# Kernel optimization log

Measured on AMD Instinct MI355X. Metric: run time of the kernel, lower is better.

Reference implementation:

```python
import jax, jax.numpy as jnp
import numpy as np

C_S, C_Z, N_HEADS = 768, 64, 12
HEAD_DIM = C_S // N_HEADS
L = 1024
EPS = 1e-5


def _ln(x, g, b):
    mu = jnp.mean(x, axis=-1, keepdims=True)
    var = jnp.mean((x - mu) ** 2, axis=-1, keepdims=True)
    return (x - mu) * jax.lax.rsqrt(var + EPS) * g + b


def setup_inputs() -> dict:
    key = jax.random.key(0)
    ks = jax.random.split(key, 12)
    w = lambda k, shp, fan_in: jax.random.normal(k, shp, dtype=jnp.float32) / np.sqrt(fan_in)
    return {
        "single": jax.random.normal(ks[0], (L, C_S), dtype=jnp.float32),
        "pair": jax.random.normal(ks[1], (L, L, C_Z), dtype=jnp.float32),
        "ln_s_g": jnp.ones((C_S,), jnp.float32),
        "ln_s_b": jnp.zeros((C_S,), jnp.float32),
        "ln_z_g": jnp.ones((C_Z,), jnp.float32),
        "ln_z_b": jnp.zeros((C_Z,), jnp.float32),
        "Wq": w(ks[2], (C_S, C_S), C_S),
        "Wk": w(ks[3], (C_S, C_S), C_S),
        "Wv": w(ks[4], (C_S, C_S), C_S),
        "Wb": w(ks[5], (C_Z, N_HEADS), C_Z),
        "Wout": w(ks[6], (C_S, C_S), C_S),
        "bout": jnp.zeros((C_S,), jnp.float32),
        "Wgate": w(ks[7], (C_S, C_S), C_S),
        "bgate": jnp.zeros((C_S,), jnp.float32),
    }


def reference(single, pair, ln_s_g, ln_s_b, ln_z_g, ln_z_b,
              Wq, Wk, Wv, Wb, Wout, bout, Wgate, bgate):
    Lq = single.shape[0]
    s = _ln(single, ln_s_g, ln_s_b)                    # [L, C_S]
    z = _ln(pair, ln_z_g, ln_z_b)                      # [L, L, C_Z]
    q = (s @ Wq).reshape(Lq, N_HEADS, HEAD_DIM)
    k = (s @ Wk).reshape(Lq, N_HEADS, HEAD_DIM)
    v = (s @ Wv).reshape(Lq, N_HEADS, HEAD_DIM)
    logits = jnp.einsum('ihd,jhd->hij', q, k) / np.sqrt(HEAD_DIM)
    logits = logits + jnp.einsum('ijc,ch->hij', z, Wb)  # pair bias per head
    attn = jax.nn.softmax(logits, axis=-1)              # [H, L, L]
    out = jnp.einsum('hij,jhd->ihd', attn, v).reshape(Lq, C_S)
    return single + jax.nn.sigmoid(s @ Wgate + bgate) * (out @ Wout + bout)
```

## Files before the change

### kernel.cpp

```cpp
#include <hip/hip_runtime.h>

#define LQ 1024
#define CS 768
#define CZ 64
#define NH 12
#define HD 64

typedef float4 f4;
using bf16x8 = __attribute__((ext_vector_type(8))) short;
using f32x4  = __attribute__((ext_vector_type(4))) float;

static __device__ __forceinline__ unsigned short f2bf(float f) {
  unsigned int u = __float_as_uint(f);
  u += 0x7fffu + ((u >> 16) & 1u);
  return (unsigned short)(u >> 16);
}
static __device__ __forceinline__ float bf2f(unsigned short b) {
  return __uint_as_float(((unsigned int)b) << 16);
}
static __device__ __forceinline__ unsigned cvtpk(float lo, float hi) {
  unsigned r;
  asm("v_cvt_pk_bf16_f32 %0, %1, %2" : "=v"(r) : "v"(lo), "v"(hi));
  return r;
}

__global__ __launch_bounds__(256) void ln_wconv_k(
    const float* __restrict__ x, const float* __restrict__ g,
    const float* __restrict__ b, unsigned short* __restrict__ s_out,
    const float* __restrict__ Wq, const float* __restrict__ Wk,
    const float* __restrict__ Wv, const float* __restrict__ Wg,
    const float* __restrict__ Wo, unsigned short* __restrict__ wt) {
  const int bid = blockIdx.x;
  const int t = threadIdx.x;
  if (bid < LQ) {
    const int row = bid;
    const float* xr = x + (size_t)row * CS;
    float v0 = xr[t], v1 = xr[t + 256], v2 = xr[t + 512];
    float s1 = v0 + v1 + v2;
    float s2 = v0 * v0 + v1 * v1 + v2 * v2;
#pragma unroll
    for (int m = 1; m < 64; m <<= 1) {
      s1 += __shfl_xor(s1, m);
      s2 += __shfl_xor(s2, m);
    }
    __shared__ float r1[4], r2[4];
    const int wid = t >> 6;
    if ((t & 63) == 0) { r1[wid] = s1; r2[wid] = s2; }
    __syncthreads();
    s1 = r1[0] + r1[1] + r1[2] + r1[3];
    s2 = r2[0] + r2[1] + r2[2] + r2[3];
    const float mu = s1 * (1.f / CS);
    const float var = s2 * (1.f / CS) - mu * mu;
    const float rs = rsqrtf(var + 1e-5f);
    s_out[(size_t)row * CS + t]       = f2bf((v0 - mu) * rs * g[t]       + b[t]);
    s_out[(size_t)row * CS + t + 256] = f2bf((v1 - mu) * rs * g[t + 256] + b[t + 256]);
    s_out[(size_t)row * CS + t + 512] = f2bf((v2 - mu) * rs * g[t + 512] + b[t + 512]);
  } else {
    int r = bid - LQ;
    const int bz = r / 144; r %= 144;
    const int n0 = (r % 12) * 64, k0 = (r / 12) * 64;
    const float* W;
    switch (bz) {
      case 0: W = Wq; break;
      case 1: W = Wk; break;
      case 2: W = Wv; break;
      case 3: W = Wg; break;
      default: W = Wo; break;
    }
    unsigned short* o = wt + (size_t)bz * CS * CS;
    __shared__ float T[64][68];
    {
      const int rr = t >> 4, c = (t & 15) * 4;
#pragma unroll
      for (int u = 0; u < 4; ++u) {
        const f4 v = *(const f4*)&W[(size_t)(k0 + rr + u * 16) * CS + n0 + c];
        *(f4*)&T[rr + u * 16][c] = v;
      }
    }
    __syncthreads();
    {
      const int rn = t >> 2, ck = (t & 3) * 16;
      __align__(16) unsigned short tmp[16];
#pragma unroll
      for (int u = 0; u < 16; ++u) tmp[u] = f2bf(T[ck + u][rn]);
      unsigned short* dst = &o[(size_t)(n0 + rn) * CS + k0 + ck];
      *(uint4*)dst = ((const uint4*)tmp)[0];
      *(uint4*)(dst + 8) = ((const uint4*)tmp)[1];
    }
  }
}

__global__ __launch_bounds__(256) void pair_k(
    const float* __restrict__ pair, const float* __restrict__ zg,
    const float* __restrict__ zb, const float* __restrict__ Wb,
    unsigned short* __restrict__ biasF) {
  __shared__ __align__(16) unsigned short outT[12 * 520 + 8];
  const int bid = blockIdx.x;
  const int t = threadIdx.x;
  const int w = t >> 6, lane = t & 63, g = lane >> 4, c = lane & 15;
  const int i0 = (bid >> 3) * 4;
  const int j0 = (bid & 7) * 128;
  const int il = c & 3, jl = c >> 2;
  const int irow = i0 + il;
  const int g2 = g * 2;

  const int csafe = (c < NH) ? c : 0;
  float C1 = 0.f, C2 = 0.f;
  for (int ch = 0; ch < CZ; ++ch) {
    const float wv = (c < NH) ? Wb[ch * NH + csafe] : 0.f;
    C1 = fmaf(zg[ch], wv, C1);
    C2 = fmaf(zb[ch], wv, C2);
  }
  bf16x8 wf0, wf1;
#pragma unroll
  for (int u = 0; u < 8; ++u) {
    const float w0 = (c < NH) ? zg[g * 8 + u] * Wb[(g * 8 + u) * NH + csafe] : 0.f;
    const float w1 = (c < NH) ? zg[32 + g * 8 + u] * Wb[(32 + g * 8 + u) * NH + csafe] : 0.f;
    wf0[u] = (short)f2bf(w0);
    wf1[u] = (short)f2bf(w1);
  }

  f32x4 p00, p01, p02, p03;
  f32x4 p10, p11, p12, p13;
  {
    const f32x4* s0 = (const f32x4*)(pair + ((size_t)irow * LQ + (j0 + w * 32 + jl)) * CZ);
    p00 = s0[g2]; p01 = s0[g2 + 1]; p02 = s0[g2 + 8]; p03 = s0[g2 + 9];
  }
#pragma unroll
  for (int it = 0; it < 8; ++it) {
    const bool useA = (it & 1) == 0;
    if (it < 7) {
      const f32x4* sn = (const f32x4*)(pair + ((size_t)irow * LQ + (j0 + w * 32 + (it + 1) * 4 + jl)) * CZ);
      if (useA) { p10 = sn[g2]; p11 = sn[g2 + 1]; p12 = sn[g2 + 8]; p13 = sn[g2 + 9]; }
      else      { p00 = sn[g2]; p01 = sn[g2 + 1]; p02 = sn[g2 + 8]; p03 = sn[g2 + 9]; }
    }
    const f32x4 x0a = useA ? p00 : p10;
    const f32x4 x0b = useA ? p01 : p11;
    const f32x4 x1a = useA ? p02 : p12;
    const f32x4 x1b = useA ? p03 : p13;

    float s1 = (((x0a[0] + x0a[1]) + (x0a[2] + x0a[3])) + ((x0b[0] + x0b[1]) + (x0b[2] + x0b[3])))
             + (((x1a[0] + x1a[1]) + (x1a[2] + x1a[3])) + ((x1b[0] + x1b[1]) + (x1b[2] + x1b[3])));
    float s2 = (((x0a[0]*x0a[0] + x0a[1]*x0a[1]) + (x0a[2]*x0a[2] + x0a[3]*x0a[3]))
             +  ((x0b[0]*x0b[0] + x0b[1]*x0b[1]) + (x0b[2]*x0b[2] + x0b[3]*x0b[3])))
             + (((x1a[0]*x1a[0] + x1a[1]*x1a[1]) + (x1a[2]*x1a[2] + x1a[3]*x1a[3]))
             +  ((x1b[0]*x1b[0] + x1b[1]*x1b[1]) + (x1b[2]*x1b[2] + x1b[3]*x1b[3])));
    s1 += __shfl_xor(s1, 16); s1 += __shfl_xor(s1, 32);
    s2 += __shfl_xor(s2, 16); s2 += __shfl_xor(s2, 32);
    const float mu = s1 * (1.f / CZ);
    const float var = s2 * (1.f / CZ) - mu * mu;
    const float rs = rsqrtf(var + 1e-5f);
    const float mup = -rs * mu;

    union { unsigned u[4]; bf16x8 v8; } A, B;
    A.u[0] = cvtpk(x0a[0], x0a[1]); A.u[1] = cvtpk(x0a[2], x0a[3]);
    A.u[2] = cvtpk(x0b[0], x0b[1]); A.u[3] = cvtpk(x0b[2], x0b[3]);
    B.u[0] = cvtpk(x1a[0], x1a[1]); B.u[1] = cvtpk(x1a[2], x1a[3]);
    B.u[2] = cvtpk(x1b[0], x1b[1]); B.u[3] = cvtpk(x1b[2], x1b[3]);

    f32x4 dd = (f32x4){0.f, 0.f, 0.f, 0.f};
    dd = __builtin_amdgcn_mfma_f32_16x16x32_bf16(A.v8, wf0, dd, 0, 0, 0);
    dd = __builtin_amdgcn_mfma_f32_16x16x32_bf16(B.v8, wf1, dd, 0, 0, 0);

    const float rr0 = __shfl(rs, g * 4 + 0), mm0 = __shfl(mup, g * 4 + 0);
    const float rr1 = __shfl(rs, g * 4 + 1), mm1 = __shfl(mup, g * 4 + 1);
    const float rr2 = __shfl(rs, g * 4 + 2), mm2 = __shfl(mup, g * 4 + 2);
    const float rr3 = __shfl(rs, g * 4 + 3), mm3 = __shfl(mup, g * 4 + 3);

    if (c < NH) {
      const float b0 = fmaf(rr0, dd[0], fmaf(mm0, C1, C2));
      const float b1 = fmaf(rr1, dd[1], fmaf(mm1, C1, C2));
      const float b2 = fmaf(rr2, dd[2], fmaf(mm2, C1, C2));
      const float b3 = fmaf(rr3, dd[3], fmaf(mm3, C1, C2));
      const int jrel = w * 32 + it * 4 + g;
      const int s = jrel >> 4;
      uint2 st;
      st.x = cvtpk(b0, b1);
      st.y = cvtpk(b2, b3);
      *(uint2*)&outT[c * 520 + s * 64 + (jrel & 15) * 4] = st;
    }
  }
  __syncthreads();

  const int gi = i0 >> 4, ga = (i0 >> 2) & 3;
#pragma unroll
  for (int rep = 0; rep < 3; ++rep) {
    const int idx = rep * 256 + t;
    const int hh = idx >> 6;
    const int s = (idx >> 3) & 7;
    const int sub = idx & 7;
    const uint4 v = *(const uint4*)&outT[hh * 520 + s * 64 + sub * 8];
    const size_t flat = ((((size_t)hh * 64 + gi) * 16 + (j0 >> 6) + (s >> 2)) * 4 + (s & 3)) * 256
                      + (size_t)ga * 64 + sub * 8;
    *(uint4*)&biasF[flat] = v;
  }
}

__global__ __launch_bounds__(256) void gemm_qkvg_k(
    const unsigned short* __restrict__ s, const unsigned short* __restrict__ wt,
    const float* __restrict__ bg,
    unsigned short* __restrict__ qb, unsigned short* __restrict__ kb,
    unsigned short* __restrict__ vt, float* __restrict__ gpre) {
  __shared__ __align__(16) unsigned short As[64][88];
  __shared__ __align__(16) unsigned short Bs[128][88];
  const int t = threadIdx.x;
  const int w = t >> 6, lane = t & 63, g = lane >> 4, c = lane & 15;
  const int wm = w >> 1, wn = w & 1;
  const int bx = blockIdx.x % 24, by = blockIdx.x / 24;
  const int m0 = by * 64;
  const int wid = bx / 6;
  const int nl0 = (bx % 6) * 128;
  const unsigned short* B = wt + (size_t)wid * CS * CS;

  f32x4 acc[2][4];
#pragma unroll
  for (int i = 0; i < 2; ++i)
#pragma unroll
    for (int j = 0; j < 4; ++j) acc[i][j] = (f32x4){0.f, 0.f, 0.f, 0.f};

  const int sra = t >> 2, sha = (t & 3) * 16;
  const int srb = t >> 1, shb = (t & 1) * 32;
  for (int kt = 0; kt < CS; kt += 64) {
    __syncthreads();
#pragma unroll
    for (int u = 0; u < 2; ++u)
      *(uint4*)&As[sra][sha + u * 8] = *(const uint4*)&s[(size_t)(m0 + sra) * CS + kt + sha + u * 8];
#pragma unroll
    for (int u = 0; u < 4; ++u)
      *(uint4*)&Bs[srb][shb + u * 8] = *(const uint4*)&B[(size_t)(nl0 + srb) * CS + kt + shb + u * 8];
    __syncthreads();
#pragma unroll
    for (int kk = 0; kk < 64; kk += 32) {
      bf16x8 af[2], bfr[4];
#pragma unroll
      for (int i = 0; i < 2; ++i) af[i] = *(const bf16x8*)&As[wm * 32 + i * 16 + c][kk + g * 8];
#pragma unroll
      for (int j = 0; j < 4; ++j) bfr[j] = *(const bf16x8*)&Bs[wn * 64 + j * 16 + c][kk + g * 8];
#pragma unroll
      for (int i = 0; i < 2; ++i)
#pragma unroll
        for (int j = 0; j < 4; ++j)
          acc[i][j] = __builtin_amdgcn_mfma_f32_16x16x32_bf16(af[i], bfr[j], acc[i][j], 0, 0, 0);
    }
  }
#pragma unroll
  for (int i = 0; i < 2; ++i) {
#pragma unroll
    for (int j = 0; j < 4; ++j) {
      const int mb = m0 + wm * 32 + i * 16 + g * 4;
      const int nn = nl0 + wn * 64 + j * 16 + c;
      const f32x4 a = acc[i][j];
      if (wid == 0) {
#pragma unroll
        for (int r = 0; r < 4; ++r) qb[(size_t)(mb + r) * CS + nn] = f2bf(a[r] * 0.125f);
      } else if (wid == 1) {
#pragma unroll
        for (int r = 0; r < 4; ++r) kb[(size_t)(mb + r) * CS + nn] = f2bf(a[r]);
      } else if (wid == 2) {
        ushort4 pk;
        pk.x = f2bf(a[0]); pk.y = f2bf(a[1]); pk.z = f2bf(a[2]); pk.w = f2bf(a[3]);
        *(ushort4*)&vt[(size_t)nn * LQ + mb] = pk;
      } else {
        const float bb = bg[nn];
#pragma unroll
        for (int r = 0; r < 4; ++r) gpre[(size_t)(mb + r) * CS + nn] = a[r] + bb;
      }
    }
  }
}

__global__ __launch_bounds__(256) void attn_k(
    const unsigned short* __restrict__ q, const unsigned short* __restrict__ k,
    const unsigned short* __restrict__ vt, const unsigned short* __restrict__ biasF,
    float* __restrict__ Opart, float* __restrict__ ml) {
  __shared__ __align__(16) unsigned short Qs[64][88];
  __shared__ __align__(16) unsigned short Ks[2][64][88];
  __shared__ __align__(16) unsigned short Vts[2][64][88];
  __shared__ __align__(16) unsigned short Ps[4][16][88];
  const int bx = blockIdx.x, h = blockIdx.y, z = blockIdx.z;
  const int i0 = bx * 64;
  const int jb = z * 512;
  const int t = threadIdx.x;
  const int w = t >> 6, lane = t & 63, g = lane >> 4, c = lane & 15;
  const int sr = t >> 2, sc = (t & 3) * 16;

#pragma unroll
  for (int u = 0; u < 2; ++u) {
    *(uint4*)&Qs[sr][sc + u * 8]     = *(const uint4*)&q[(size_t)(i0 + sr) * CS + h * HD + sc + u * 8];
    *(uint4*)&Ks[0][sr][sc + u * 8]  = *(const uint4*)&k[(size_t)(jb + sr) * CS + h * HD + sc + u * 8];
    *(uint4*)&Vts[0][sr][sc + u * 8] = *(const uint4*)&vt[(size_t)(h * HD + sr) * LQ + jb + sc + u * 8];
  }
  const size_t bbase = ((((size_t)h * 64 + (bx * 4 + w)) * 16 + (size_t)z * 8) * 4) * 256 + lane * 4;
  ushort4 bcur[4];
#pragma unroll
  for (int nb = 0; nb < 4; ++nb) bcur[nb] = *(const ushort4*)&biasF[bbase + nb * 256];
  __syncthreads();

  const bf16x8 aq0 = *(const bf16x8*)&Qs[w * 16 + c][g * 8];
  const bf16x8 aq1 = *(const bf16x8*)&Qs[w * 16 + c][32 + g * 8];

  f32x4 acc_o[4];
#pragma unroll
  for (int nb = 0; nb < 4; ++nb) acc_o[nb] = (f32x4){0.f, 0.f, 0.f, 0.f};
  float m_run[4] = {-1e30f, -1e30f, -1e30f, -1e30f};
  float l_run[4] = {0.f, 0.f, 0.f, 0.f};

  for (int jt = 0; jt < 8; ++jt) {
    const int cur = jt & 1;
    uint4 kr0, kr1, vr0, vr1;
    ushort4 bnx[4];
    if (jt < 7) {
      const int jn = jb + (jt + 1) * 64;
      kr0 = *(const uint4*)&k[(size_t)(jn + sr) * CS + h * HD + sc];
      kr1 = *(const uint4*)&k[(size_t)(jn + sr) * CS + h * HD + sc + 8];
      vr0 = *(const uint4*)&vt[(size_t)(h * HD + sr) * LQ + jn + sc];
      vr1 = *(const uint4*)&vt[(size_t)(h * HD + sr) * LQ + jn + sc + 8];
#pragma unroll
      for (int nb = 0; nb < 4; ++nb)
        bnx[nb] = *(const ushort4*)&biasF[bbase + (size_t)(jt + 1) * 1024 + nb * 256];
    }

    f32x4 sa[4];
#pragma unroll
    for (int nb = 0; nb < 4; ++nb) {
      f32x4 ci;
      ci[0] = bf2f(bcur[nb].x); ci[1] = bf2f(bcur[nb].y);
      ci[2] = bf2f(bcur[nb].z); ci[3] = bf2f(bcur[nb].w);
      const bf16x8 b0 = *(const bf16x8*)&Ks[cur][nb * 16 + c][g * 8];
      const bf16x8 b1 = *(const bf16x8*)&Ks[cur][nb * 16 + c][32 + g * 8];
      ci = __builtin_amdgcn_mfma_f32_16x16x32_bf16(aq0, b0, ci, 0, 0, 0);
      ci = __builtin_amdgcn_mfma_f32_16x16x32_bf16(aq1, b1, ci, 0, 0, 0);
      sa[nb] = ci;
    }

    float mt[4];
#pragma unroll
    for (int r = 0; r < 4; ++r) {
      float v = fmaxf(fmaxf(sa[0][r], sa[1][r]), fmaxf(sa[2][r], sa[3][r]));
      v = fmaxf(v, __shfl_xor(v, 1));
      v = fmaxf(v, __shfl_xor(v, 2));
      v = fmaxf(v, __shfl_xor(v, 4));
      v = fmaxf(v, __shfl_xor(v, 8));
      mt[r] = v;
    }
    float scale[4], ps[4];
#pragma unroll
    for (int r = 0; r < 4; ++r) {
      const float mn = fmaxf(m_run[r], mt[r]);
      scale[r] = __expf(m_run[r] - mn);
      m_run[r] = mn;
      ps[r] = 0.f;
    }
#pragma unroll
    for (int nb = 0; nb < 4; ++nb) {
#pragma unroll
      for (int r = 0; r < 4; ++r) {
        const float p = __expf(sa[nb][r] - m_run[r]);
        ps[r] += p;
        Ps[w][g * 4 + r][nb * 16 + c] = f2bf(p);
      }
    }
#pragma unroll
    for (int r = 0; r < 4; ++r) {
      float v = ps[r];
      v += __shfl_xor(v, 1);
      v += __shfl_xor(v, 2);
      v += __shfl_xor(v, 4);
      v += __shfl_xor(v, 8);
      l_run[r] = l_run[r] * scale[r] + v;
#pragma unroll
      for (int nb = 0; nb < 4; ++nb) acc_o[nb][r] *= scale[r];
    }

#pragma unroll
    for (int kb = 0; kb < 2; ++kb) {
      const bf16x8 pa = *(const bf16x8*)&Ps[w][c][kb * 32 + g * 8];
#pragma unroll
      for (int nb = 0; nb < 4; ++nb) {
        const bf16x8 bv = *(const bf16x8*)&Vts[cur][nb * 16 + c][kb * 32 + g * 8];
        acc_o[nb] = __builtin_amdgcn_mfma_f32_16x16x32_bf16(pa, bv, acc_o[nb], 0, 0, 0);
      }
    }

    if (jt < 7) {
      *(uint4*)&Ks[cur ^ 1][sr][sc]      = kr0;
      *(uint4*)&Ks[cur ^ 1][sr][sc + 8]  = kr1;
      *(uint4*)&Vts[cur ^ 1][sr][sc]     = vr0;
      *(uint4*)&Vts[cur ^ 1][sr][sc + 8] = vr1;
      __syncthreads();
#pragma unroll
      for (int nb = 0; nb < 4; ++nb) bcur[nb] = bnx[nb];
    }
  }

  const size_t rowb = (size_t)(z * NH + h) * LQ + i0 + w * 16 + g * 4;
#pragma unroll
  for (int nb = 0; nb < 4; ++nb)
#pragma unroll
    for (int r = 0; r < 4; ++r)
      Opart[(rowb + r) * HD + nb * 16 + c] = acc_o[nb][r];
  if (c == 0) {
#pragma unroll
    for (int r = 0; r < 4; ++r) {
      ml[(rowb + r) * 2]     = m_run[r];
      ml[(rowb + r) * 2 + 1] = l_run[r];
    }
  }
}

__global__ __launch_bounds__(256) void combine_k(
    const float* __restrict__ Opart, const float* __restrict__ ml,
    unsigned short* __restrict__ attno) {
  const int t = threadIdx.x;
  const int row = blockIdx.x * 4 + (t >> 6);
  const int d = t & 63;
  const int h = row >> 10, i = row & 1023;
  const size_t r0 = (size_t)h * LQ + i;
  const size_t r1 = (size_t)(NH + h) * LQ + i;
  const float m0 = ml[r0 * 2], l0 = ml[r0 * 2 + 1];
  const float m1 = ml[r1 * 2], l1 = ml[r1 * 2 + 1];
  const float M = fmaxf(m0, m1);
  const float a0 = __expf(m0 - M), a1 = __expf(m1 - M);
  const float L = a0 * l0 + a1 * l1;
  const float o = (a0 * Opart[r0 * HD + d] + a1 * Opart[r1 * HD + d]) / L;
  attno[(size_t)i * CS + h * HD + d] = f2bf(o);
}

__global__ __launch_bounds__(256) void gemm_final_k(
    const unsigned short* __restrict__ A, const unsigned short* __restrict__ wt,
    const float* __restrict__ bout, const float* __restrict__ single,
    const float* __restrict__ gpre, float* __restrict__ out) {
  __shared__ __align__(16) unsigned short As[64][88];
  __shared__ __align__(16) unsigned short Bs[128][88];
  const int t = threadIdx.x;
  const int wave = t >> 6, lane = t & 63, g = lane >> 4, c = lane & 15;
  const int wm = wave >> 1, wn = wave & 1;
  const int m0 = blockIdx.y * 64;
  const int nl0 = blockIdx.x * 128;
  const unsigned short* B = wt + (size_t)4 * CS * CS;

  f32x4 acc[2][4];
#pragma unroll
  for (int i = 0; i < 2; ++i)
#pragma unroll
    for (int j = 0; j < 4; ++j) acc[i][j] = (f32x4){0.f, 0.f, 0.f, 0.f};

  const int sra = t >> 2, sha = (t & 3) * 16;
  const int srb = t >> 1, shb = (t & 1) * 32;
  for (int kt = 0; kt < CS; kt += 64) {
    __syncthreads();
#pragma unroll
    for (int u = 0; u < 2; ++u)
      *(uint4*)&As[sra][sha + u * 8] = *(const uint4*)&A[(size_t)(m0 + sra) * CS + kt + sha + u * 8];
#pragma unroll
    for (int u = 0; u < 4; ++u)
      *(uint4*)&Bs[srb][shb + u * 8] = *(const uint4*)&B[(size_t)(nl0 + srb) * CS + kt + shb + u * 8];
    __syncthreads();
#pragma unroll
    for (int kk = 0; kk < 64; kk += 32) {
      bf16x8 af[2], bfr[4];
#pragma unroll
      for (int i = 0; i < 2; ++i) af[i] = *(const bf16x8*)&As[wm * 32 + i * 16 + c][kk + g * 8];
#pragma unroll
      for (int j = 0; j < 4; ++j) bfr[j] = *(const bf16x8*)&Bs[wn * 64 + j * 16 + c][kk + g * 8];
#pragma unroll
      for (int i = 0; i < 2; ++i)
#pragma unroll
        for (int j = 0; j < 4; ++j)
          acc[i][j] = __builtin_amdgcn_mfma_f32_16x16x32_bf16(af[i], bfr[j], acc[i][j], 0, 0, 0);
    }
  }

#pragma unroll
  for (int i = 0; i < 2; ++i) {
#pragma unroll
    for (int j = 0; j < 4; ++j) {
      const int mb = m0 + wm * 32 + i * 16 + g * 4;
      const int nn = nl0 + wn * 64 + j * 16 + c;
      const float bb = bout[nn];
      const f32x4 a = acc[i][j];
#pragma unroll
      for (int r = 0; r < 4; ++r) {
        const size_t idx = (size_t)(mb + r) * CS + nn;
        const float gate = 1.f / (1.f + __expf(-gpre[idx]));
        out[idx] = single[idx] + gate * (a[r] + bb);
      }
    }
  }
}

extern "C" void kernel_launch(void* const* d_in, const int* in_sizes, int n_in,
                              void* d_out, int out_size, void* d_ws, size_t ws_size,
                              hipStream_t stream) {
  const float* single = (const float*)d_in[0];
  const float* pair   = (const float*)d_in[1];
  const float* ln_s_g = (const float*)d_in[2];
  const float* ln_s_b = (const float*)d_in[3];
  const float* ln_z_g = (const float*)d_in[4];
  const float* ln_z_b = (const float*)d_in[5];
  const float* Wq     = (const float*)d_in[6];
  const float* Wk     = (const float*)d_in[7];
  const float* Wv     = (const float*)d_in[8];
  const float* Wb     = (const float*)d_in[9];
  const float* Wout   = (const float*)d_in[10];
  const float* bout   = (const float*)d_in[11];
  const float* Wgate  = (const float*)d_in[12];
  const float* bgate  = (const float*)d_in[13];
  float* out = (float*)d_out;

  unsigned short* s_bf  = (unsigned short*)d_ws;
  unsigned short* wt    = s_bf  + (size_t)LQ * CS;
  unsigned short* q_bf  = wt    + (size_t)5 * CS * CS;
  unsigned short* k_bf  = q_bf  + (size_t)LQ * CS;
  unsigned short* vt_bf = k_bf  + (size_t)LQ * CS;
  unsigned short* attno = vt_bf + (size_t)CS * LQ;
  unsigned short* biasF = attno + (size_t)LQ * CS;
  float* gpre  = (float*)(biasF + (size_t)NH * LQ * LQ);
  float* Opart = gpre  + (size_t)LQ * CS;
  float* mlw   = Opart + (size_t)2 * NH * LQ * HD;

  hipLaunchKernelGGL(pair_k, dim3(2048), dim3(256), 0, stream,
                     pair, ln_z_g, ln_z_b, Wb, biasF);
  hipLaunchKernelGGL(ln_wconv_k, dim3(LQ + 720), dim3(256), 0, stream,
                     single, ln_s_g, ln_s_b, s_bf, Wq, Wk, Wv, Wgate, Wout, wt);
  hipLaunchKernelGGL(gemm_qkvg_k, dim3(384), dim3(256), 0, stream,
                     s_bf, wt, bgate, q_bf, k_bf, vt_bf, gpre);
  hipLaunchKernelGGL(attn_k, dim3(16, NH, 2), dim3(256), 0, stream,
                     q_bf, k_bf, vt_bf, biasF, Opart, mlw);
  hipLaunchKernelGGL(combine_k, dim3(3072), dim3(256), 0, stream,
                     Opart, mlw, attno);
  hipLaunchKernelGGL(gemm_final_k, dim3(6, 16), dim3(256), 0, stream,
                     attno, wt, bout, single, gpre, out);
}
```

Measured before the change: 121.2 us.

## Merge pair-bias and QKVG GEMM kernels into one heterogeneous launch

```diff
diff --git a/kernel.cpp b/kernel.cpp
--- a/kernel.cpp
+++ b/kernel.cpp
@@ -90,180 +90,181 @@
   }
 }
 
-__global__ __launch_bounds__(256) void pair_k(
+__global__ __launch_bounds__(256) void qkvg_pair_k(
+    const unsigned short* __restrict__ s, const unsigned short* __restrict__ wt,
+    const float* __restrict__ bg,
+    unsigned short* __restrict__ qb, unsigned short* __restrict__ kb,
+    unsigned short* __restrict__ vt, float* __restrict__ gpre,
     const float* __restrict__ pair, const float* __restrict__ zg,
     const float* __restrict__ zb, const float* __restrict__ Wb,
     unsigned short* __restrict__ biasF) {
-  __shared__ __align__(16) unsigned short outT[12 * 520 + 8];
+  __shared__ __align__(16) unsigned short sm[64 * 88 + 128 * 88];
   const int bid = blockIdx.x;
   const int t = threadIdx.x;
   const int w = t >> 6, lane = t & 63, g = lane >> 4, c = lane & 15;
-  const int i0 = (bid >> 3) * 4;
-  const int j0 = (bid & 7) * 128;
-  const int il = c & 3, jl = c >> 2;
-  const int irow = i0 + il;
-  const int g2 = g * 2;
-
-  const int csafe = (c < NH) ? c : 0;
-  float C1 = 0.f, C2 = 0.f;
-  for (int ch = 0; ch < CZ; ++ch) {
-    const float wv = (c < NH) ? Wb[ch * NH + csafe] : 0.f;
-    C1 = fmaf(zg[ch], wv, C1);
-    C2 = fmaf(zb[ch], wv, C2);
-  }
-  bf16x8 wf0, wf1;
-#pragma unroll
-  for (int u = 0; u < 8; ++u) {
-    const float w0 = (c < NH) ? zg[g * 8 + u] * Wb[(g * 8 + u) * NH + csafe] : 0.f;
-    const float w1 = (c < NH) ? zg[32 + g * 8 + u] * Wb[(32 + g * 8 + u) * NH + csafe] : 0.f;
-    wf0[u] = (short)f2bf(w0);
-    wf1[u] = (short)f2bf(w1);
-  }
-
-  f32x4 p00, p01, p02, p03;
-  f32x4 p10, p11, p12, p13;
-  {
-    const f32x4* s0 = (const f32x4*)(pair + ((size_t)irow * LQ + (j0 + w * 32 + jl)) * CZ);
-    p00 = s0[g2]; p01 = s0[g2 + 1]; p02 = s0[g2 + 8]; p03 = s0[g2 + 9];
-  }
-#pragma unroll
-  for (int it = 0; it < 8; ++it) {
-    const bool useA = (it & 1) == 0;
-    if (it < 7) {
-      const f32x4* sn = (const f32x4*)(pair + ((size_t)irow * LQ + (j0 + w * 32 + (it + 1) * 4 + jl)) * CZ);
-      if (useA) { p10 = sn[g2]; p11 = sn[g2 + 1]; p12 = sn[g2 + 8]; p13 = sn[g2 + 9]; }
-      else      { p00 = sn[g2]; p01 = sn[g2 + 1]; p02 = sn[g2 + 8]; p03 = sn[g2 + 9]; }
-    }
-    const f32x4 x0a = useA ? p00 : p10;
-    const f32x4 x0b = useA ? p01 : p11;
-    const f32x4 x1a = useA ? p02 : p12;
-    const f32x4 x1b = useA ? p03 : p13;
-
-    float s1 = (((x0a[0] + x0a[1]) + (x0a[2] + x0a[3])) + ((x0b[0] + x0b[1]) + (x0b[2] + x0b[3])))
-             + (((x1a[0] + x1a[1]) + (x1a[2] + x1a[3])) + ((x1b[0] + x1b[1]) + (x1b[2] + x1b[3])));
-    float s2 = (((x0a[0]*x0a[0] + x0a[1]*x0a[1]) + (x0a[2]*x0a[2] + x0a[3]*x0a[3]))
-             +  ((x0b[0]*x0b[0] + x0b[1]*x0b[1]) + (x0b[2]*x0b[2] + x0b[3]*x0b[3])))
-             + (((x1a[0]*x1a[0] + x1a[1]*x1a[1]) + (x1a[2]*x1a[2] + x1a[3]*x1a[3]))
-             +  ((x1b[0]*x1b[0] + x1b[1]*x1b[1]) + (x1b[2]*x1b[2] + x1b[3]*x1b[3])));
-    s1 += __shfl_xor(s1, 16); s1 += __shfl_xor(s1, 32);
-    s2 += __shfl_xor(s2, 16); s2 += __shfl_xor(s2, 32);
-    const float mu = s1 * (1.f / CZ);
-    const float var = s2 * (1.f / CZ) - mu * mu;
-    const float rs = rsqrtf(var + 1e-5f);
-    const float mup = -rs * mu;
-
-    union { unsigned u[4]; bf16x8 v8; } A, B;
-    A.u[0] = cvtpk(x0a[0], x0a[1]); A.u[1] = cvtpk(x0a[2], x0a[3]);
-    A.u[2] = cvtpk(x0b[0], x0b[1]); A.u[3] = cvtpk(x0b[2], x0b[3]);
-    B.u[0] = cvtpk(x1a[0], x1a[1]); B.u[1] = cvtpk(x1a[2], x1a[3]);
-    B.u[2] = cvtpk(x1b[0], x1b[1]); B.u[3] = cvtpk(x1b[2], x1b[3]);
-
-    f32x4 dd = (f32x4){0.f, 0.f, 0.f, 0.f};
-    dd = __builtin_amdgcn_mfma_f32_16x16x32_bf16(A.v8, wf0, dd, 0, 0, 0);
-    dd = __builtin_amdgcn_mfma_f32_16x16x32_bf16(B.v8, wf1, dd, 0, 0, 0);
-
-    const float rr0 = __shfl(rs, g * 4 + 0), mm0 = __shfl(mup, g * 4 + 0);
-    const float rr1 = __shfl(rs, g * 4 + 1), mm1 = __shfl(mup, g * 4 + 1);
-    const float rr2 = __shfl(rs, g * 4 + 2), mm2 = __shfl(mup, g * 4 + 2);
-    const float rr3 = __shfl(rs, g * 4 + 3), mm3 = __shfl(mup, g * 4 + 3);
-
-    if (c < NH) {
-      const float b0 = fmaf(rr0, dd[0], fmaf(mm0, C1, C2));
-      const float b1 = fmaf(rr1, dd[1], fmaf(mm1, C1, C2));
-      const float b2 = fmaf(rr2, dd[2], fmaf(mm2, C1, C2));
-      const float b3 = fmaf(rr3, dd[3], fmaf(mm3, C1, C2));
-      const int jrel = w * 32 + it * 4 + g;
-      const int s = jrel >> 4;
-      uint2 st;
-      st.x = cvtpk(b0, b1);
-      st.y = cvtpk(b2, b3);
-      *(uint2*)&outT[c * 520 + s * 64 + (jrel & 15) * 4] = st;
-    }
-  }
-  __syncthreads();
-
-  const int gi = i0 >> 4, ga = (i0 >> 2) & 3;
-#pragma unroll
-  for (int rep = 0; rep < 3; ++rep) {
-    const int idx = rep * 256 + t;
-    const int hh = idx >> 6;
-    const int s = (idx >> 3) & 7;
-    const int sub = idx & 7;
-    const uint4 v = *(const uint4*)&outT[hh * 520 + s * 64 + sub * 8];
-    const size_t flat = ((((size_t)hh * 64 + gi) * 16 + (j0 >> 6) + (s >> 2)) * 4 + (s & 3)) * 256
-                      + (size_t)ga * 64 + sub * 8;
-    *(uint4*)&biasF[flat] = v;
-  }
-}
-
-__global__ __launch_bounds__(256) void gemm_qkvg_k(
-    const unsigned short* __restrict__ s, const unsigned short* __restrict__ wt,
-    const float* __restrict__ bg,
-    unsigned short* __restrict__ qb, unsigned short* __restrict__ kb,
-    unsigned short* __restrict__ vt, float* __restrict__ gpre) {
-  __shared__ __align__(16) unsigned short As[64][88];
-  __shared__ __align__(16) unsigned short Bs[128][88];
-  const int t = threadIdx.x;
-  const int w = t >> 6, lane = t & 63, g = lane >> 4, c = lane & 15;
-  const int wm = w >> 1, wn = w & 1;
-  const int bx = blockIdx.x % 24, by = blockIdx.x / 24;
-  const int m0 = by * 64;
-  const int wid = bx / 6;
-  const int nl0 = (bx % 6) * 128;
-  const unsigned short* B = wt + (size_t)wid * CS * CS;
-
-  f32x4 acc[2][4];
-#pragma unroll
-  for (int i = 0; i < 2; ++i)
-#pragma unroll
-    for (int j = 0; j < 4; ++j) acc[i][j] = (f32x4){0.f, 0.f, 0.f, 0.f};
-
-  const int sra = t >> 2, sha = (t & 3) * 16;
-  const int srb = t >> 1, shb = (t & 1) * 32;
-  for (int kt = 0; kt < CS; kt += 64) {
+
+  if (bid < 2048) {
+    unsigned short* outT = sm;
+    const int i0 = (bid >> 3) * 4;
+    const int j0 = (bid & 7) * 128;
+    const int il = c & 3, jl = c >> 2;
+    const int irow = i0 + il;
+    const int g2 = g * 2;
+
+    const int csafe = (c < NH) ? c : 0;
+    float C1 = 0.f, C2 = 0.f;
+    for (int ch = 0; ch < CZ; ++ch) {
+      const float wv = (c < NH) ? Wb[ch * NH + csafe] : 0.f;
+      C1 = fmaf(zg[ch], wv, C1);
+      C2 = fmaf(zb[ch], wv, C2);
+    }
+    bf16x8 wf0, wf1;
+#pragma unroll
+    for (int u = 0; u < 8; ++u) {
+      const float w0 = (c < NH) ? zg[g * 8 + u] * Wb[(g * 8 + u) * NH + csafe] : 0.f;
+      const float w1 = (c < NH) ? zg[32 + g * 8 + u] * Wb[(32 + g * 8 + u) * NH + csafe] : 0.f;
+      wf0[u] = (short)f2bf(w0);
+      wf1[u] = (short)f2bf(w1);
+    }
+
+    f32x4 p00, p01, p02, p03;
+    f32x4 p10, p11, p12, p13;
+    {
+      const f32x4* s0 = (const f32x4*)(pair + ((size_t)irow * LQ + (j0 + w * 32 + jl)) * CZ);
+      p00 = s0[g2]; p01 = s0[g2 + 1]; p02 = s0[g2 + 8]; p03 = s0[g2 + 9];
+    }
+#pragma unroll
+    for (int it = 0; it < 8; ++it) {
+      const bool useA = (it & 1) == 0;
+      if (it < 7) {
+        const f32x4* sn = (const f32x4*)(pair + ((size_t)irow * LQ + (j0 + w * 32 + (it + 1) * 4 + jl)) * CZ);
+        if (useA) { p10 = sn[g2]; p11 = sn[g2 + 1]; p12 = sn[g2 + 8]; p13 = sn[g2 + 9]; }
+        else      { p00 = sn[g2]; p01 = sn[g2 + 1]; p02 = sn[g2 + 8]; p03 = sn[g2 + 9]; }
+      }
+      const f32x4 x0a = useA ? p00 : p10;
+      const f32x4 x0b = useA ? p01 : p11;
+      const f32x4 x1a = useA ? p02 : p12;
+      const f32x4 x1b = useA ? p03 : p13;
+
+      float s1 = (((x0a[0] + x0a[1]) + (x0a[2] + x0a[3])) + ((x0b[0] + x0b[1]) + (x0b[2] + x0b[3])))
+               + (((x1a[0] + x1a[1]) + (x1a[2] + x1a[3])) + ((x1b[0] + x1b[1]) + (x1b[2] + x1b[3])));
+      float s2 = (((x0a[0]*x0a[0] + x0a[1]*x0a[1]) + (x0a[2]*x0a[2] + x0a[3]*x0a[3]))
+               +  ((x0b[0]*x0b[0] + x0b[1]*x0b[1]) + (x0b[2]*x0b[2] + x0b[3]*x0b[3])))
+               + (((x1a[0]*x1a[0] + x1a[1]*x1a[1]) + (x1a[2]*x1a[2] + x1a[3]*x1a[3]))
+               +  ((x1b[0]*x1b[0] + x1b[1]*x1b[1]) + (x1b[2]*x1b[2] + x1b[3]*x1b[3])));
+      s1 += __shfl_xor(s1, 16); s1 += __shfl_xor(s1, 32);
+      s2 += __shfl_xor(s2, 16); s2 += __shfl_xor(s2, 32);
+      const float mu = s1 * (1.f / CZ);
+      const float var = s2 * (1.f / CZ) - mu * mu;
+      const float rs = rsqrtf(var + 1e-5f);
+      const float mup = -rs * mu;
+
+      union { unsigned u[4]; bf16x8 v8; } A, B;
+      A.u[0] = cvtpk(x0a[0], x0a[1]); A.u[1] = cvtpk(x0a[2], x0a[3]);
+      A.u[2] = cvtpk(x0b[0], x0b[1]); A.u[3] = cvtpk(x0b[2], x0b[3]);
+      B.u[0] = cvtpk(x1a[0], x1a[1]); B.u[1] = cvtpk(x1a[2], x1a[3]);
+      B.u[2] = cvtpk(x1b[0], x1b[1]); B.u[3] = cvtpk(x1b[2], x1b[3]);
+
+      f32x4 dd = (f32x4){0.f, 0.f, 0.f, 0.f};
+      dd = __builtin_amdgcn_mfma_f32_16x16x32_bf16(A.v8, wf0, dd, 0, 0, 0);
+      dd = __builtin_amdgcn_mfma_f32_16x16x32_bf16(B.v8, wf1, dd, 0, 0, 0);
+
+      const float rr0 = __shfl(rs, g * 4 + 0), mm0 = __shfl(mup, g * 4 + 0);
+      const float rr1 = __shfl(rs, g * 4 + 1), mm1 = __shfl(mup, g * 4 + 1);
+      const float rr2 = __shfl(rs, g * 4 + 2), mm2 = __shfl(mup, g * 4 + 2);
+      const float rr3 = __shfl(rs, g * 4 + 3), mm3 = __shfl(mup, g * 4 + 3);
+
+      if (c < NH) {
+        const float b0 = fmaf(rr0, dd[0], fmaf(mm0, C1, C2));
+        const float b1 = fmaf(rr1, dd[1], fmaf(mm1, C1, C2));
+        const float b2 = fmaf(rr2, dd[2], fmaf(mm2, C1, C2));
+        const float b3 = fmaf(rr3, dd[3], fmaf(mm3, C1, C2));
+        const int jrel = w * 32 + it * 4 + g;
+        const int sp = jrel >> 4;
+        uint2 st;
+        st.x = cvtpk(b0, b1);
+        st.y = cvtpk(b2, b3);
+        *(uint2*)&outT[c * 520 + sp * 64 + (jrel & 15) * 4] = st;
+      }
+    }
     __syncthreads();
-#pragma unroll
-    for (int u = 0; u < 2; ++u)
-      *(uint4*)&As[sra][sha + u * 8] = *(const uint4*)&s[(size_t)(m0 + sra) * CS + kt + sha + u * 8];
-#pragma unroll
-    for (int u = 0; u < 4; ++u)
-      *(uint4*)&Bs[srb][shb + u * 8] = *(const uint4*)&B[(size_t)(nl0 + srb) * CS + kt + shb + u * 8];
-    __syncthreads();
-#pragma unroll
-    for (int kk = 0; kk < 64; kk += 32) {
-      bf16x8 af[2], bfr[4];
-#pragma unroll
-      for (int i = 0; i < 2; ++i) af[i] = *(const bf16x8*)&As[wm * 32 + i * 16 + c][kk + g * 8];
-#pragma unroll
-      for (int j = 0; j < 4; ++j) bfr[j] = *(const bf16x8*)&Bs[wn * 64 + j * 16 + c][kk + g * 8];
-#pragma unroll
-      for (int i = 0; i < 2; ++i)
-#pragma unroll
-        for (int j = 0; j < 4; ++j)
-          acc[i][j] = __builtin_amdgcn_mfma_f32_16x16x32_bf16(af[i], bfr[j], acc[i][j], 0, 0, 0);
-    }
-  }
-#pragma unroll
-  for (int i = 0; i < 2; ++i) {
-#pragma unroll
-    for (int j = 0; j < 4; ++j) {
-      const int mb = m0 + wm * 32 + i * 16 + g * 4;
-      const int nn = nl0 + wn * 64 + j * 16 + c;
-      const f32x4 a = acc[i][j];
-      if (wid == 0) {
-#pragma unroll
-        for (int r = 0; r < 4; ++r) qb[(size_t)(mb + r) * CS + nn] = f2bf(a[r] * 0.125f);
-      } else if (wid == 1) {
-#pragma unroll
-        for (int r = 0; r < 4; ++r) kb[(size_t)(mb + r) * CS + nn] = f2bf(a[r]);
-      } else if (wid == 2) {
-        ushort4 pk;
-        pk.x = f2bf(a[0]); pk.y = f2bf(a[1]); pk.z = f2bf(a[2]); pk.w = f2bf(a[3]);
-        *(ushort4*)&vt[(size_t)nn * LQ + mb] = pk;
-      } else {
-        const float bb = bg[nn];
-#pragma unroll
-        for (int r = 0; r < 4; ++r) gpre[(size_t)(mb + r) * CS + nn] = a[r] + bb;
+
+    const int gi = i0 >> 4, ga = (i0 >> 2) & 3;
+#pragma unroll
+    for (int rep = 0; rep < 3; ++rep) {
+      const int idx = rep * 256 + t;
+      const int hh = idx >> 6;
+      const int sp = (idx >> 3) & 7;
+      const int sub = idx & 7;
+      const uint4 v = *(const uint4*)&outT[hh * 520 + sp * 64 + sub * 8];
+      const size_t flat = ((((size_t)hh * 64 + gi) * 16 + (j0 >> 6) + (sp >> 2)) * 4 + (sp & 3)) * 256
+                        + (size_t)ga * 64 + sub * 8;
+      *(uint4*)&biasF[flat] = v;
+    }
+  } else {
+    unsigned short (*As)[88] = (unsigned short (*)[88])sm;
+    unsigned short (*Bs)[88] = (unsigned short (*)[88])(sm + 64 * 88);
+    const int gb = bid - 2048;
+    const int wm = w >> 1, wn = w & 1;
+    const int bx = gb % 24, by = gb / 24;
+    const int m0 = by * 64;
+    const int wid = bx / 6;
+    const int nl0 = (bx % 6) * 128;
+    const unsigned short* B = wt + (size_t)wid * CS * CS;
+
+    f32x4 acc[2][4];
+#pragma unroll
+    for (int i = 0; i < 2; ++i)
+#pragma unroll
+      for (int j = 0; j < 4; ++j) acc[i][j] = (f32x4){0.f, 0.f, 0.f, 0.f};
+
+    const int sra = t >> 2, sha = (t & 3) * 16;
+    const int srb = t >> 1, shb = (t & 1) * 32;
+    for (int kt = 0; kt < CS; kt += 64) {
+      __syncthreads();
+#pragma unroll
+      for (int u = 0; u < 2; ++u)
+        *(uint4*)&As[sra][sha + u * 8] = *(const uint4*)&s[(size_t)(m0 + sra) * CS + kt + sha + u * 8];
+#pragma unroll
+      for (int u = 0; u < 4; ++u)
+        *(uint4*)&Bs[srb][shb + u * 8] = *(const uint4*)&B[(size_t)(nl0 + srb) * CS + kt + shb + u * 8];
+      __syncthreads();
+#pragma unroll
+      for (int kk = 0; kk < 64; kk += 32) {
+        bf16x8 af[2], bfr[4];
+#pragma unroll
+        for (int i = 0; i < 2; ++i) af[i] = *(const bf16x8*)&As[wm * 32 + i * 16 + c][kk + g * 8];
+#pragma unroll
+        for (int j = 0; j < 4; ++j) bfr[j] = *(const bf16x8*)&Bs[wn * 64 + j * 16 + c][kk + g * 8];
+#pragma unroll
+        for (int i = 0; i < 2; ++i)
+#pragma unroll
+          for (int j = 0; j < 4; ++j)
+            acc[i][j] = __builtin_amdgcn_mfma_f32_16x16x32_bf16(af[i], bfr[j], acc[i][j], 0, 0, 0);
+      }
+    }
+#pragma unroll
+    for (int i = 0; i < 2; ++i) {
+#pragma unroll
+      for (int j = 0; j < 4; ++j) {
+        const int mb = m0 + wm * 32 + i * 16 + g * 4;
+        const int nn = nl0 + wn * 64 + j * 16 + c;
+        const f32x4 a = acc[i][j];
+        if (wid == 0) {
+#pragma unroll
+          for (int r = 0; r < 4; ++r) qb[(size_t)(mb + r) * CS + nn] = f2bf(a[r] * 0.125f);
+        } else if (wid == 1) {
+#pragma unroll
+          for (int r = 0; r < 4; ++r) kb[(size_t)(mb + r) * CS + nn] = f2bf(a[r]);
+        } else if (wid == 2) {
+          ushort4 pk;
+          pk.x = f2bf(a[0]); pk.y = f2bf(a[1]); pk.z = f2bf(a[2]); pk.w = f2bf(a[3]);
+          *(ushort4*)&vt[(size_t)nn * LQ + mb] = pk;
+        } else {
+          const float bb = bg[nn];
+#pragma unroll
+          for (int r = 0; r < 4; ++r) gpre[(size_t)(mb + r) * CS + nn] = a[r] + bb;
+        }
       }
     }
   }
@@ -519,12 +520,11 @@
   float* Opart = gpre  + (size_t)LQ * CS;
   float* mlw   = Opart + (size_t)2 * NH * LQ * HD;
 
-  hipLaunchKernelGGL(pair_k, dim3(2048), dim3(256), 0, stream,
-                     pair, ln_z_g, ln_z_b, Wb, biasF);
   hipLaunchKernelGGL(ln_wconv_k, dim3(LQ + 720), dim3(256), 0, stream,
                      single, ln_s_g, ln_s_b, s_bf, Wq, Wk, Wv, Wgate, Wout, wt);
-  hipLaunchKernelGGL(gemm_qkvg_k, dim3(384), dim3(256), 0, stream,
-                     s_bf, wt, bgate, q_bf, k_bf, vt_bf, gpre);
+  hipLaunchKernelGGL(qkvg_pair_k, dim3(2048 + 384), dim3(256), 0, stream,
+                     s_bf, wt, bgate, q_bf, k_bf, vt_bf, gpre,
+                     pair, ln_z_g, ln_z_b, Wb, biasF);
   hipLaunchKernelGGL(attn_k, dim3(16, NH, 2), dim3(256), 0, stream,
                      q_bf, k_bf, vt_bf, biasF, Opart, mlw);
   hipLaunchKernelGGL(combine_k, dim3(3072), dim3(256), 0, stream,
```

New measurement: 119.9 us (median of 2 runs). Within noise of the previous version (-1.1%).
